# Optimization experiments

Hardware: AMD Instinct MI355X
Metric: run time of the kernel (lower is better)

## Reference

```python
import jax, jax.numpy as jnp
import numpy as np

N_HEADS = 16
D_QK = 64
D_MODEL = 1024
LN_EPS = 1e-6
B, QL, KVL = 2, 2048, 2048


def rms_norm(x, weight, eps=LN_EPS):
    var = jnp.mean(jnp.square(x.astype(jnp.float32)), axis=-1, keepdims=True)
    return (x * jax.lax.rsqrt(var + eps)).astype(x.dtype) * weight


def setup_inputs() -> dict:
    key = jax.random.key(0)
    ks = jax.random.split(key, 5)
    scale_h = 1.0 / np.sqrt(D_MODEL)
    return {
        "q_hidden_states": jax.random.normal(ks[0], (B, QL, D_MODEL), jnp.float32),
        "q_sequence_mask": jnp.ones((B, QL), dtype=bool),
        "kv_hidden_states": jax.random.normal(ks[1], (B, KVL, D_MODEL), jnp.float32),
        "kv_sequence_mask": jnp.ones((B, KVL), dtype=bool),
        "w_q": jax.random.normal(ks[2], (D_MODEL, N_HEADS * D_QK), jnp.float32) * scale_h,
        "w_kv": jax.random.normal(ks[3], (D_MODEL, 2 * N_HEADS * D_QK), jnp.float32) * scale_h,
        "w_o": jax.random.normal(ks[4], (N_HEADS * D_QK, D_MODEL), jnp.float32) * scale_h,
        "ln_weight": jnp.ones((D_MODEL,), jnp.float32),
    }


def reference(q_hidden_states, q_sequence_mask, kv_hidden_states, kv_sequence_mask,
              w_q, w_kv, w_o, ln_weight):
    b, ql, _ = q_hidden_states.shape
    kvl = kv_hidden_states.shape[1]

    normed = rms_norm(q_hidden_states, ln_weight)

    # q projection: [b, ql, H*D] -> [b, H, ql, D]
    q = (normed @ w_q).reshape(b, ql, N_HEADS, D_QK).transpose(0, 2, 1, 3)
    # kv projection: [b, kvl, 2*H*D] -> k, v each [b, H, kvl, D]
    kv = (kv_hidden_states @ w_kv).reshape(b, kvl, 2, N_HEADS, D_QK)
    k = kv[:, :, 0].transpose(0, 2, 1, 3)
    v = kv[:, :, 1].transpose(0, 2, 1, 3)

    # T5 attention: no 1/sqrt(d) scaling
    scores = jnp.einsum("bhqd,bhkd->bhqk", q, k)  # [b, H, ql, kvl]
    attn_mask = q_sequence_mask[:, None, :, None] & kv_sequence_mask[:, None, None, :]
    scores = jnp.where(attn_mask, scores, jnp.finfo(jnp.float32).min)
    attn = jax.nn.softmax(scores.astype(jnp.float32), axis=-1).astype(q.dtype)

    out = jnp.einsum("bhqk,bhkd->bhqd", attn, v)  # [b, H, ql, D]
    out = out.transpose(0, 2, 1, 3).reshape(b, ql, N_HEADS * D_QK)
    out = out @ w_o
    return q_hidden_states + out
```

## Files before the change

### kernel.cpp

```cpp
#include <hip/hip_runtime.h>
#include <stdint.h>

#define BSZ 2
#define QL 2048
#define KVL 2048
#define NH 16
#define DQK 64
#define DM 1024

typedef __bf16 bf16x8 __attribute__((ext_vector_type(8)));
typedef float f32x4 __attribute__((ext_vector_type(4)));

__device__ __forceinline__ ushort f2bf(float f) {
    union { float f; uint32_t u; } c; c.f = f;
    uint32_t u = c.u;
    return (ushort)((u + 0x7fffu + ((u >> 16) & 1u)) >> 16);
}

__device__ __forceinline__ uint32_t pack2bf(float lo, float hi) {
    union { float f; uint32_t u; } a, b;
    a.f = lo; b.f = hi;
    return __builtin_amdgcn_perm(b.u + 0x8000u, a.u + 0x8000u, 0x07060302u);
}

#define GLOAD_LDS16(g, l)                                              \
    __builtin_amdgcn_global_load_lds(                                  \
        (const __attribute__((address_space(1))) uint32_t*)(g),        \
        (__attribute__((address_space(3))) uint32_t*)(l), 16, 0, 0)

__global__ __launch_bounds__(256) void rmsnorm_cast_k(const float* __restrict__ x,
                                                      const float* __restrict__ w,
                                                      ushort* __restrict__ out) {
    int row = blockIdx.x;
    const float4* xr = (const float4*)(x + (size_t)row * DM);
    float4 v = xr[threadIdx.x];
    float s = v.x * v.x + v.y * v.y + v.z * v.z + v.w * v.w;
#pragma unroll
    for (int off = 32; off > 0; off >>= 1) s += __shfl_down(s, off, 64);
    __shared__ float ws4[4];
    if ((threadIdx.x & 63) == 0) ws4[threadIdx.x >> 6] = s;
    __syncthreads();
    float tot = ws4[0] + ws4[1] + ws4[2] + ws4[3];
    float r = rsqrtf(tot * (1.0f / DM) + 1e-6f);
    float4 wv = ((const float4*)w)[threadIdx.x];
    ushort4 o;
    o.x = f2bf(v.x * r * wv.x);
    o.y = f2bf(v.y * r * wv.y);
    o.z = f2bf(v.z * r * wv.z);
    o.w = f2bf(v.w * r * wv.w);
    ((ushort4*)(out + (size_t)row * DM))[threadIdx.x] = o;
}

__global__ __launch_bounds__(256) void prep_k(const float* __restrict__ kv_in,
                                              ushort* __restrict__ kvb,
                                              const float* __restrict__ w_q,
                                              const float* __restrict__ w_kv,
                                              const float* __restrict__ w_o,
                                              ushort* __restrict__ wqT,
                                              ushort* __restrict__ wkvT,
                                              ushort* __restrict__ woT) {
    __shared__ ushort tile[64][65];
    int blk = blockIdx.x;
    int tid = threadIdx.x;
    if (blk < 4096) {
        int i = blk * 256 + tid;
        float4 v = ((const float4*)kv_in)[i];
        ushort4 r;
        r.x = f2bf(v.x); r.y = f2bf(v.y); r.z = f2bf(v.z); r.w = f2bf(v.w);
        ((ushort4*)kvb)[i] = r;
        return;
    }
    int bi = blk - 4096;
    const float* in; ushort* out; int N, bx, by;
    const int K = 1024;
    if (bi < 256)      { in = w_q;  out = wqT;  N = 1024; bx = bi & 15; by = bi >> 4; }
    else if (bi < 768) { int j = bi - 256; in = w_kv; out = wkvT; N = 2048; bx = j & 31; by = j >> 5; }
    else               { int j = bi - 768; in = w_o;  out = woT;  N = 1024; bx = j & 15; by = j >> 4; }
    int k0 = by * 64, n0 = bx * 64;
    int colBase = tid & 63;
    int rowOff = tid >> 6;
#pragma unroll
    for (int i = 0; i < 16; ++i) {
        int row = i * 4 + rowOff;
        tile[colBase][row] = f2bf(in[(size_t)(k0 + row) * N + n0 + colBase]);
    }
    __syncthreads();
#pragma unroll
    for (int i = 0; i < 16; ++i) {
        int nrow = i * 4 + rowOff;
        out[(size_t)(n0 + nrow) * K + k0 + colBase] = tile[nrow][colBase];
    }
}

__global__ __launch_bounds__(256) void transpose_v_k(const ushort* __restrict__ v,
                                                     ushort* __restrict__ vt) {
    int bh = blockIdx.y;
    int t0 = blockIdx.x * 64;
    int lane = threadIdx.x & 63, wave = threadIdx.x >> 6;
    const ushort* src = v + (size_t)bh * KVL * DQK;
    ushort* dst = vt + (size_t)bh * DQK * KVL;
    int t = t0 + lane;
    int tp = (t & ~28) | ((t & 16) >> 2) | ((t & 4) << 1) | ((t & 8) << 1);
#pragma unroll
    for (int it = 0; it < 2; ++it) {
        int d0 = (wave * 2 + it) * 8;
        union { uint4 u; ushort s[8]; } val;
        val.u = *(const uint4*)&src[(size_t)t * DQK + d0];
#pragma unroll
        for (int j = 0; j < 8; ++j)
            dst[(size_t)(d0 + j) * KVL + tp] = val.s[j];
    }
}

__global__ __launch_bounds__(256) void gemm_qkv_k(
    const ushort* __restrict__ normed, const ushort* __restrict__ kvb,
    const ushort* __restrict__ wqT, const ushort* __restrict__ wkvT,
    ushort* __restrict__ q_out, ushort* __restrict__ k_out, ushort* __restrict__ v_out) {
    __shared__ __align__(16) ushort As[128 * 32];
    __shared__ __align__(16) ushort Bs[128 * 32];
    const int K = DM;
    int tid = threadIdx.x;
    int wave = tid >> 6, lane = tid & 63, quad = lane >> 4, l16 = lane & 15;
    int bx = blockIdx.x;
    int isQ = bx < 8;
    const ushort* A = isQ ? normed : kvb;
    const ushort* Bt = isQ ? wqT : wkvT;
    int n0 = (isQ ? bx : bx - 8) * 128;
    int m0 = blockIdx.y * 128;
    int wm = (wave & 1) * 64, wn = (wave >> 1) * 64;

    int r0 = tid >> 2, c0 = (tid & 3) << 3;
    const ushort* ga0 = &A[(size_t)(m0 + r0) * K + c0];
    const ushort* gb0 = &Bt[(size_t)(n0 + r0) * K + c0];

    f32x4 zero = {0.f, 0.f, 0.f, 0.f};
    f32x4 acc[4][4];
#pragma unroll
    for (int i = 0; i < 4; ++i)
#pragma unroll
        for (int j = 0; j < 4; ++j) acc[i][j] = zero;

    for (int k0 = 0; k0 < K; k0 += 32) {
        GLOAD_LDS16(ga0 + k0, &As[tid * 8]);
        GLOAD_LDS16(ga0 + (size_t)64 * K + k0, &As[(tid + 256) * 8]);
        GLOAD_LDS16(gb0 + k0, &Bs[tid * 8]);
        GLOAD_LDS16(gb0 + (size_t)64 * K + k0, &Bs[(tid + 256) * 8]);
        __syncthreads();
        bf16x8 af[4], bfr[4];
#pragma unroll
        for (int mi = 0; mi < 4; ++mi)
            af[mi] = *(const bf16x8*)(&As[(wm + mi * 16 + l16) * 32 + quad * 8]);
#pragma unroll
        for (int ni = 0; ni < 4; ++ni)
            bfr[ni] = *(const bf16x8*)(&Bs[(wn + ni * 16 + l16) * 32 + quad * 8]);
#pragma unroll
        for (int mi = 0; mi < 4; ++mi)
#pragma unroll
            for (int ni = 0; ni < 4; ++ni)
                acc[mi][ni] = __builtin_amdgcn_mfma_f32_16x16x32_bf16(
                    af[mi], bfr[ni], acc[mi][ni], 0, 0, 0);
        __syncthreads();
    }

    const float L2E = 1.44269504089f;
#pragma unroll
    for (int mi = 0; mi < 4; ++mi) {
#pragma unroll
        for (int ni = 0; ni < 4; ++ni) {
#pragma unroll
            for (int r = 0; r < 4; ++r) {
                int mm = m0 + wm + mi * 16 + quad * 4 + r;
                int nn = n0 + wn + ni * 16 + l16;
                float val = acc[mi][ni][r];
                int b = mm >> 11, t = mm & 2047;
                if (isQ) {
                    int h = nn >> 6, d = nn & 63;
                    q_out[((size_t)((b << 4) | h) * QL + t) * DQK + d] = f2bf(val * L2E);
                } else {
                    int c = nn >> 10, h = (nn >> 6) & 15, d = nn & 63;
                    ushort* dst = c ? v_out : k_out;
                    dst[((size_t)((b << 4) | h) * KVL + t) * DQK + d] = f2bf(val);
                }
            }
        }
    }
}

__global__ __launch_bounds__(256) void gemm_o_k(const ushort* __restrict__ A,
                                                const ushort* __restrict__ Bt,
                                                const float* __restrict__ resid,
                                                float* __restrict__ f_out) {
    __shared__ __align__(16) ushort As[64 * 32];
    __shared__ __align__(16) ushort Bs[128 * 32];
    const int K = DM;
    int tid = threadIdx.x;
    int wave = tid >> 6, lane = tid & 63, quad = lane >> 4, l16 = lane & 15;
    int n0 = blockIdx.x * 128, m0 = blockIdx.y * 64;
    int wm = (wave & 1) * 32, wn = (wave >> 1) * 64;

    int r0 = tid >> 2, c0 = (tid & 3) << 3;
    const ushort* ga0 = &A[(size_t)(m0 + r0) * K + c0];
    const ushort* gb0 = &Bt[(size_t)(n0 + r0) * K + c0];

    f32x4 zero = {0.f, 0.f, 0.f, 0.f};
    f32x4 acc[2][4];
#pragma unroll
    for (int i = 0; i < 2; ++i)
#pragma unroll
        for (int j = 0; j < 4; ++j) acc[i][j] = zero;

    for (int k0 = 0; k0 < K; k0 += 32) {
        GLOAD_LDS16(ga0 + k0, &As[tid * 8]);
        GLOAD_LDS16(gb0 + k0, &Bs[tid * 8]);
        GLOAD_LDS16(gb0 + (size_t)64 * K + k0, &Bs[(tid + 256) * 8]);
        __syncthreads();
        bf16x8 af[2], bfr[4];
#pragma unroll
        for (int mi = 0; mi < 2; ++mi)
            af[mi] = *(const bf16x8*)(&As[(wm + mi * 16 + l16) * 32 + quad * 8]);
#pragma unroll
        for (int ni = 0; ni < 4; ++ni)
            bfr[ni] = *(const bf16x8*)(&Bs[(wn + ni * 16 + l16) * 32 + quad * 8]);
#pragma unroll
        for (int mi = 0; mi < 2; ++mi)
#pragma unroll
            for (int ni = 0; ni < 4; ++ni)
                acc[mi][ni] = __builtin_amdgcn_mfma_f32_16x16x32_bf16(
                    af[mi], bfr[ni], acc[mi][ni], 0, 0, 0);
        __syncthreads();
    }

#pragma unroll
    for (int mi = 0; mi < 2; ++mi) {
#pragma unroll
        for (int ni = 0; ni < 4; ++ni) {
#pragma unroll
            for (int r = 0; r < 4; ++r) {
                int mm = m0 + wm + mi * 16 + quad * 4 + r;
                int nn = n0 + wn + ni * 16 + l16;
                size_t o = (size_t)mm * DM + nn;
                f_out[o] = resid[o] + acc[mi][ni][r];
            }
        }
    }
}

__global__ __launch_bounds__(256) void attn_k(const ushort* __restrict__ qh,
                                              const ushort* __restrict__ kh,
                                              const ushort* __restrict__ vt,
                                              ushort* __restrict__ ao) {
    __shared__ __align__(16) ushort smem[2 * 64 * 72];
    ushort* Ks = smem;
    ushort* Vs = smem + 64 * 72;
    int bh = blockIdx.y, bI = bh >> 4, hI = bh & 15;
    int q0 = blockIdx.x * 128;
    int tid = threadIdx.x, wave = tid >> 6, lane = tid & 63;
    int quad = lane >> 4, l16 = lane & 15;
    const ushort* Qp = qh + (size_t)bh * QL * DQK;
    const ushort* Kp = kh + (size_t)bh * KVL * DQK;
    const ushort* Vp = vt + (size_t)bh * DQK * KVL;

    bf16x8 qf[2][2];
#pragma unroll
    for (int g = 0; g < 2; ++g) {
        const ushort* qrow = Qp + (size_t)(q0 + wave * 32 + g * 16 + l16) * DQK;
        qf[g][0] = *(const bf16x8*)(qrow + quad * 8);
        qf[g][1] = *(const bf16x8*)(qrow + 32 + quad * 8);
    }

    int srow = tid >> 3;
    int scol = (tid & 7) << 3;

    f32x4 zero = {0.f, 0.f, 0.f, 0.f};
    f32x4 o[2][4];
#pragma unroll
    for (int g = 0; g < 2; ++g)
#pragma unroll
        for (int i = 0; i < 4; ++i) o[g][i] = zero;
    float lsum[2] = {0.f, 0.f};

    uint4 kr0 = *(const uint4*)&Kp[(size_t)srow * DQK + scol];
    uint4 kr1 = *(const uint4*)&Kp[(size_t)(srow + 32) * DQK + scol];
    uint4 vr0 = *(const uint4*)&Vp[(size_t)srow * KVL + scol];
    uint4 vr1 = *(const uint4*)&Vp[(size_t)(srow + 32) * KVL + scol];

    for (int t0 = 0; t0 < KVL; t0 += 64) {
        *(uint4*)&Ks[srow * 72 + scol] = kr0;
        *(uint4*)&Ks[(srow + 32) * 72 + scol] = kr1;
        *(uint4*)&Vs[srow * 72 + scol] = vr0;
        *(uint4*)&Vs[(srow + 32) * 72 + scol] = vr1;
        __syncthreads();
        int tn = t0 + 64;
        if (tn < KVL) {
            kr0 = *(const uint4*)&Kp[(size_t)(tn + srow) * DQK + scol];
            kr1 = *(const uint4*)&Kp[(size_t)(tn + srow + 32) * DQK + scol];
            vr0 = *(const uint4*)&Vp[(size_t)srow * KVL + tn + scol];
            vr1 = *(const uint4*)&Vp[(size_t)(srow + 32) * KVL + tn + scol];
        }

        f32x4 s[2][4];
#pragma unroll
        for (int mi = 0; mi < 4; ++mi) {
            const ushort* kb = &Ks[(mi * 16 + l16) * 72 + quad * 8];
            bf16x8 kf0 = *(const bf16x8*)kb;
            bf16x8 kf1 = *(const bf16x8*)(kb + 32);
#pragma unroll
            for (int g = 0; g < 2; ++g) {
                f32x4 a = zero;
                a = __builtin_amdgcn_mfma_f32_16x16x32_bf16(kf0, qf[g][0], a, 0, 0, 0);
                a = __builtin_amdgcn_mfma_f32_16x16x32_bf16(kf1, qf[g][1], a, 0, 0, 0);
                s[g][mi] = a;
            }
        }

        bf16x8 pf[2][2];
#pragma unroll
        for (int g = 0; g < 2; ++g) {
            float rs = 0.f;
            uint32_t pw[8];
#pragma unroll
            for (int mi = 0; mi < 4; ++mi) {
                float e0 = __builtin_amdgcn_exp2f(s[g][mi][0]);
                float e1 = __builtin_amdgcn_exp2f(s[g][mi][1]);
                float e2 = __builtin_amdgcn_exp2f(s[g][mi][2]);
                float e3 = __builtin_amdgcn_exp2f(s[g][mi][3]);
                rs += (e0 + e1) + (e2 + e3);
                asm("v_cvt_pk_bf16_f32 %0, %1, %2" : "=v"(pw[mi * 2]) : "v"(e0), "v"(e1));
                asm("v_cvt_pk_bf16_f32 %0, %1, %2" : "=v"(pw[mi * 2 + 1]) : "v"(e2), "v"(e3));
            }
            lsum[g] += rs;
            union { uint32_t u[4]; bf16x8 v; } b0, b1;
            b0.u[0] = pw[0]; b0.u[1] = pw[1]; b0.u[2] = pw[2]; b0.u[3] = pw[3];
            b1.u[0] = pw[4]; b1.u[1] = pw[5]; b1.u[2] = pw[6]; b1.u[3] = pw[7];
            pf[g][0] = b0.v;
            pf[g][1] = b1.v;
        }

#pragma unroll
        for (int mi = 0; mi < 4; ++mi) {
            const ushort* vb = &Vs[(mi * 16 + l16) * 72 + quad * 8];
            bf16x8 vf0 = *(const bf16x8*)vb;
            bf16x8 vf1 = *(const bf16x8*)(vb + 32);
#pragma unroll
            for (int g = 0; g < 2; ++g) {
                o[g][mi] = __builtin_amdgcn_mfma_f32_16x16x32_bf16(vf0, pf[g][0], o[g][mi], 0, 0, 0);
                o[g][mi] = __builtin_amdgcn_mfma_f32_16x16x32_bf16(vf1, pf[g][1], o[g][mi], 0, 0, 0);
            }
        }
        __syncthreads();
    }

#pragma unroll
    for (int g = 0; g < 2; ++g) {
        float lg = lsum[g];
        lg += __shfl_xor(lg, 16, 64);
        lg += __shfl_xor(lg, 32, 64);
        float rinv = __builtin_amdgcn_rcpf(lg);
        ushort* orow = &smem[(size_t)(wave * 32 + g * 16 + l16) * 72];
#pragma unroll
        for (int mi = 0; mi < 4; ++mi) {
            uint2 pk;
            pk.x = pack2bf(o[g][mi][0] * rinv, o[g][mi][1] * rinv);
            pk.y = pack2bf(o[g][mi][2] * rinv, o[g][mi][3] * rinv);
            *(uint2*)&orow[mi * 16 + quad * 4] = pk;
        }
    }
    __syncthreads();
#pragma unroll
    for (int it = 0; it < 4; ++it) {
        int idx = tid + it * 256;
        int ql = idx >> 3, c = (idx & 7) << 3;
        uint4 vv = *(const uint4*)&smem[ql * 72 + c];
        *(uint4*)&ao[((size_t)(bI * QL + q0 + ql)) * DM + hI * 64 + c] = vv;
    }
}

extern "C" void kernel_launch(void* const* d_in, const int* in_sizes, int n_in,
                              void* d_out, int out_size, void* d_ws, size_t ws_size,
                              hipStream_t stream) {
    (void)in_sizes; (void)n_in; (void)out_size; (void)ws_size;
    const float* qh_in = (const float*)d_in[0];
    const float* kv_in = (const float*)d_in[2];
    const float* w_q  = (const float*)d_in[4];
    const float* w_kv = (const float*)d_in[5];
    const float* w_o  = (const float*)d_in[6];
    const float* lnw  = (const float*)d_in[7];
    float* out = (float*)d_out;

    char* ws = (char*)d_ws;
    ushort* normed = (ushort*)(ws);
    ushort* vT     = (ushort*)(ws);
    ushort* kvb    = (ushort*)(ws + ((size_t)8 << 20));
    ushort* wqT    = (ushort*)(ws + ((size_t)16 << 20));
    ushort* wkvT   = (ushort*)(ws + ((size_t)18 << 20));
    ushort* woT    = (ushort*)(ws + ((size_t)22 << 20));
    ushort* qheads = (ushort*)(ws + ((size_t)24 << 20));
    ushort* kheads = (ushort*)(ws + ((size_t)32 << 20));
    ushort* vheads = (ushort*)(ws + ((size_t)40 << 20));
    ushort* attno  = (ushort*)(ws + ((size_t)48 << 20));

    rmsnorm_cast_k<<<BSZ * QL, 256, 0, stream>>>(qh_in, lnw, normed);
    prep_k<<<4096 + 1024, 256, 0, stream>>>(kv_in, kvb, w_q, w_kv, w_o, wqT, wkvT, woT);

    gemm_qkv_k<<<dim3(24, 32), 256, 0, stream>>>(normed, kvb, wqT, wkvT,
                                                 qheads, kheads, vheads);
    transpose_v_k<<<dim3(KVL / 64, BSZ * NH), 256, 0, stream>>>(vheads, vT);
    attn_k<<<dim3(QL / 128, BSZ * NH), 256, 0, stream>>>(qheads, kheads, vT, attno);
    gemm_o_k<<<dim3(8, 64), 256, 0, stream>>>(attno, woT, qh_in, out);
}
```

Measured before the change: 207.7 us.

## Load attention K/V fragments directly from global memory, dropping LDS staging and barriers

The attention kernel no longer stages K and V tiles through shared memory with two barriers per iteration. Each wave now loads its MFMA fragments for K and V straight from global memory into registers, software-prefetching the next K tile. The goal is to remove LDS traffic and block-level synchronisation. The cost is that every wave redundantly fetches the full K/V tiles (4x more global/L2 traffic per block) and uses more registers, partly offset by a launch-bounds hint for two blocks per SIMD-group.

After: 282.3 us. 35.9% more time.

```diff
diff --git a/kernel.cpp b/kernel.cpp
--- a/kernel.cpp
+++ b/kernel.cpp
@@ -245,13 +245,11 @@
     }
 }
 
-__global__ __launch_bounds__(256) void attn_k(const ushort* __restrict__ qh,
-                                              const ushort* __restrict__ kh,
-                                              const ushort* __restrict__ vt,
-                                              ushort* __restrict__ ao) {
-    __shared__ __align__(16) ushort smem[2 * 64 * 72];
-    ushort* Ks = smem;
-    ushort* Vs = smem + 64 * 72;
+__global__ __launch_bounds__(256, 2) void attn_k(const ushort* __restrict__ qh,
+                                                 const ushort* __restrict__ kh,
+                                                 const ushort* __restrict__ vt,
+                                                 ushort* __restrict__ ao) {
+    __shared__ __align__(16) ushort smem[128 * 72];
     int bh = blockIdx.y, bI = bh >> 4, hI = bh & 15;
     int q0 = blockIdx.x * 128;
     int tid = threadIdx.x, wave = tid >> 6, lane = tid & 63;
@@ -268,8 +266,8 @@
         qf[g][1] = *(const bf16x8*)(qrow + 32 + quad * 8);
     }
 
-    int srow = tid >> 3;
-    int scol = (tid & 7) << 3;
+    const ushort* kfb = Kp + (size_t)l16 * DQK + quad * 8;
+    const ushort* vfb = Vp + (size_t)l16 * KVL + quad * 8;
 
     f32x4 zero = {0.f, 0.f, 0.f, 0.f};
     f32x4 o[2][4];
@@ -279,36 +277,37 @@
         for (int i = 0; i < 4; ++i) o[g][i] = zero;
     float lsum[2] = {0.f, 0.f};
 
-    uint4 kr0 = *(const uint4*)&Kp[(size_t)srow * DQK + scol];
-    uint4 kr1 = *(const uint4*)&Kp[(size_t)(srow + 32) * DQK + scol];
-    uint4 vr0 = *(const uint4*)&Vp[(size_t)srow * KVL + scol];
-    uint4 vr1 = *(const uint4*)&Vp[(size_t)(srow + 32) * KVL + scol];
+    bf16x8 kc[4][2], kn[4][2];
+#pragma unroll
+    for (int mi = 0; mi < 4; ++mi) {
+        kc[mi][0] = *(const bf16x8*)(kfb + (size_t)(mi * 16) * DQK);
+        kc[mi][1] = *(const bf16x8*)(kfb + (size_t)(mi * 16) * DQK + 32);
+    }
 
     for (int t0 = 0; t0 < KVL; t0 += 64) {
-        *(uint4*)&Ks[srow * 72 + scol] = kr0;
-        *(uint4*)&Ks[(srow + 32) * 72 + scol] = kr1;
-        *(uint4*)&Vs[srow * 72 + scol] = vr0;
-        *(uint4*)&Vs[(srow + 32) * 72 + scol] = vr1;
-        __syncthreads();
+        bf16x8 vc[4][2];
+#pragma unroll
+        for (int mi = 0; mi < 4; ++mi) {
+            vc[mi][0] = *(const bf16x8*)(vfb + (size_t)(mi * 16) * KVL + t0);
+            vc[mi][1] = *(const bf16x8*)(vfb + (size_t)(mi * 16) * KVL + t0 + 32);
+        }
         int tn = t0 + 64;
         if (tn < KVL) {
-            kr0 = *(const uint4*)&Kp[(size_t)(tn + srow) * DQK + scol];
-            kr1 = *(const uint4*)&Kp[(size_t)(tn + srow + 32) * DQK + scol];
-            vr0 = *(const uint4*)&Vp[(size_t)srow * KVL + tn + scol];
-            vr1 = *(const uint4*)&Vp[(size_t)(srow + 32) * KVL + tn + scol];
+#pragma unroll
+            for (int mi = 0; mi < 4; ++mi) {
+                kn[mi][0] = *(const bf16x8*)(kfb + (size_t)(tn + mi * 16) * DQK);
+                kn[mi][1] = *(const bf16x8*)(kfb + (size_t)(tn + mi * 16) * DQK + 32);
+            }
         }
 
         f32x4 s[2][4];
 #pragma unroll
         for (int mi = 0; mi < 4; ++mi) {
-            const ushort* kb = &Ks[(mi * 16 + l16) * 72 + quad * 8];
-            bf16x8 kf0 = *(const bf16x8*)kb;
-            bf16x8 kf1 = *(const bf16x8*)(kb + 32);
 #pragma unroll
             for (int g = 0; g < 2; ++g) {
                 f32x4 a = zero;
-                a = __builtin_amdgcn_mfma_f32_16x16x32_bf16(kf0, qf[g][0], a, 0, 0, 0);
-                a = __builtin_amdgcn_mfma_f32_16x16x32_bf16(kf1, qf[g][1], a, 0, 0, 0);
+                a = __builtin_amdgcn_mfma_f32_16x16x32_bf16(kc[mi][0], qf[g][0], a, 0, 0, 0);
+                a = __builtin_amdgcn_mfma_f32_16x16x32_bf16(kc[mi][1], qf[g][1], a, 0, 0, 0);
                 s[g][mi] = a;
             }
         }
@@ -338,16 +337,18 @@
 
 #pragma unroll
         for (int mi = 0; mi < 4; ++mi) {
-            const ushort* vb = &Vs[(mi * 16 + l16) * 72 + quad * 8];
-            bf16x8 vf0 = *(const bf16x8*)vb;
-            bf16x8 vf1 = *(const bf16x8*)(vb + 32);
 #pragma unroll
             for (int g = 0; g < 2; ++g) {
-                o[g][mi] = __builtin_amdgcn_mfma_f32_16x16x32_bf16(vf0, pf[g][0], o[g][mi], 0, 0, 0);
-                o[g][mi] = __builtin_amdgcn_mfma_f32_16x16x32_bf16(vf1, pf[g][1], o[g][mi], 0, 0, 0);
-            }
-        }
-        __syncthreads();
+                o[g][mi] = __builtin_amdgcn_mfma_f32_16x16x32_bf16(vc[mi][0], pf[g][0], o[g][mi], 0, 0, 0);
+                o[g][mi] = __builtin_amdgcn_mfma_f32_16x16x32_bf16(vc[mi][1], pf[g][1], o[g][mi], 0, 0, 0);
+            }
+        }
+
+#pragma unroll
+        for (int mi = 0; mi < 4; ++mi) {
+            kc[mi][0] = kn[mi][0];
+            kc[mi][1] = kn[mi][1];
+        }
     }
 
 #pragma unroll
```

## Fuse V transpose into QKV GEMM epilogue and double-buffer attention K/V tiles

Applied to the files above, without the earlier changes.

The QKV GEMM epilogue now writes V directly in the transposed, permuted layout that attention expects, packing four bf16 values per store. This removes the separate transpose kernel and one round trip of V through global memory. The attention kernel also double-buffers its K/V shared-memory tiles, so the next tile is written after compute and one barrier per iteration is dropped. In exchange, shared memory per block doubles, which may lower occupancy, and the transposed V stores from the GEMM are strided.

Result: slower. 222.7 us (+7.2%).

```diff
diff --git a/kernel.cpp b/kernel.cpp
--- a/kernel.cpp
+++ b/kernel.cpp
@@ -92,30 +92,10 @@
     }
 }
 
-__global__ __launch_bounds__(256) void transpose_v_k(const ushort* __restrict__ v,
-                                                     ushort* __restrict__ vt) {
-    int bh = blockIdx.y;
-    int t0 = blockIdx.x * 64;
-    int lane = threadIdx.x & 63, wave = threadIdx.x >> 6;
-    const ushort* src = v + (size_t)bh * KVL * DQK;
-    ushort* dst = vt + (size_t)bh * DQK * KVL;
-    int t = t0 + lane;
-    int tp = (t & ~28) | ((t & 16) >> 2) | ((t & 4) << 1) | ((t & 8) << 1);
-#pragma unroll
-    for (int it = 0; it < 2; ++it) {
-        int d0 = (wave * 2 + it) * 8;
-        union { uint4 u; ushort s[8]; } val;
-        val.u = *(const uint4*)&src[(size_t)t * DQK + d0];
-#pragma unroll
-        for (int j = 0; j < 8; ++j)
-            dst[(size_t)(d0 + j) * KVL + tp] = val.s[j];
-    }
-}
-
 __global__ __launch_bounds__(256) void gemm_qkv_k(
     const ushort* __restrict__ normed, const ushort* __restrict__ kvb,
     const ushort* __restrict__ wqT, const ushort* __restrict__ wkvT,
-    ushort* __restrict__ q_out, ushort* __restrict__ k_out, ushort* __restrict__ v_out) {
+    ushort* __restrict__ q_out, ushort* __restrict__ k_out, ushort* __restrict__ vT) {
     __shared__ __align__(16) ushort As[128 * 32];
     __shared__ __align__(16) ushort Bs[128 * 32];
     const int K = DM;
@@ -167,19 +147,29 @@
     for (int mi = 0; mi < 4; ++mi) {
 #pragma unroll
         for (int ni = 0; ni < 4; ++ni) {
-#pragma unroll
-            for (int r = 0; r < 4; ++r) {
-                int mm = m0 + wm + mi * 16 + quad * 4 + r;
-                int nn = n0 + wn + ni * 16 + l16;
-                float val = acc[mi][ni][r];
-                int b = mm >> 11, t = mm & 2047;
-                if (isQ) {
-                    int h = nn >> 6, d = nn & 63;
-                    q_out[((size_t)((b << 4) | h) * QL + t) * DQK + d] = f2bf(val * L2E);
-                } else {
-                    int c = nn >> 10, h = (nn >> 6) & 15, d = nn & 63;
-                    ushort* dst = c ? v_out : k_out;
-                    dst[((size_t)((b << 4) | h) * KVL + t) * DQK + d] = f2bf(val);
+            int nn = n0 + wn + ni * 16 + l16;
+            if (!isQ && (nn >> 10)) {
+                int h = (nn >> 6) & 15, d = nn & 63;
+                int mm0 = m0 + wm + mi * 16 + quad * 4;
+                int b = mm0 >> 11, tb = mm0 & 2047;
+                int tp = (tb & ~28) | ((tb & 16) >> 2) | ((tb & 4) << 1) | ((tb & 8) << 1);
+                uint2 pk;
+                pk.x = pack2bf(acc[mi][ni][0], acc[mi][ni][1]);
+                pk.y = pack2bf(acc[mi][ni][2], acc[mi][ni][3]);
+                *(uint2*)&vT[((size_t)((b << 4) | h) * DQK + d) * KVL + tp] = pk;
+            } else {
+#pragma unroll
+                for (int r = 0; r < 4; ++r) {
+                    int mm = m0 + wm + mi * 16 + quad * 4 + r;
+                    float val = acc[mi][ni][r];
+                    int b = mm >> 11, t = mm & 2047;
+                    if (isQ) {
+                        int h = nn >> 6, d = nn & 63;
+                        q_out[((size_t)((b << 4) | h) * QL + t) * DQK + d] = f2bf(val * L2E);
+                    } else {
+                        int h = (nn >> 6) & 15, d = nn & 63;
+                        k_out[((size_t)((b << 4) | h) * KVL + t) * DQK + d] = f2bf(val);
+                    }
                 }
             }
         }
@@ -249,9 +239,8 @@
                                               const ushort* __restrict__ kh,
                                               const ushort* __restrict__ vt,
                                               ushort* __restrict__ ao) {
-    __shared__ __align__(16) ushort smem[2 * 64 * 72];
-    ushort* Ks = smem;
-    ushort* Vs = smem + 64 * 72;
+    __shared__ __align__(16) ushort smem[4 * 64 * 72];
+    const int HALF = 64 * 72;
     int bh = blockIdx.y, bI = bh >> 4, hI = bh & 15;
     int q0 = blockIdx.x * 128;
     int tid = threadIdx.x, wave = tid >> 6, lane = tid & 63;
@@ -279,18 +268,27 @@
         for (int i = 0; i < 4; ++i) o[g][i] = zero;
     float lsum[2] = {0.f, 0.f};
 
-    uint4 kr0 = *(const uint4*)&Kp[(size_t)srow * DQK + scol];
-    uint4 kr1 = *(const uint4*)&Kp[(size_t)(srow + 32) * DQK + scol];
-    uint4 vr0 = *(const uint4*)&Vp[(size_t)srow * KVL + scol];
-    uint4 vr1 = *(const uint4*)&Vp[(size_t)(srow + 32) * KVL + scol];
-
+    {
+        uint4 a = *(const uint4*)&Kp[(size_t)srow * DQK + scol];
+        uint4 b = *(const uint4*)&Kp[(size_t)(srow + 32) * DQK + scol];
+        uint4 c = *(const uint4*)&Vp[(size_t)srow * KVL + scol];
+        uint4 d = *(const uint4*)&Vp[(size_t)(srow + 32) * KVL + scol];
+        *(uint4*)&smem[srow * 72 + scol] = a;
+        *(uint4*)&smem[(srow + 32) * 72 + scol] = b;
+        *(uint4*)&smem[HALF + srow * 72 + scol] = c;
+        *(uint4*)&smem[HALF + (srow + 32) * 72 + scol] = d;
+    }
+    __syncthreads();
+
+    int cur = 0;
     for (int t0 = 0; t0 < KVL; t0 += 64) {
-        *(uint4*)&Ks[srow * 72 + scol] = kr0;
-        *(uint4*)&Ks[(srow + 32) * 72 + scol] = kr1;
-        *(uint4*)&Vs[srow * 72 + scol] = vr0;
-        *(uint4*)&Vs[(srow + 32) * 72 + scol] = vr1;
-        __syncthreads();
+        ushort* Ks = smem + cur * 2 * HALF;
+        ushort* Vs = Ks + HALF;
+        ushort* Kn = smem + (cur ^ 1) * 2 * HALF;
+        ushort* Vn = Kn + HALF;
+
         int tn = t0 + 64;
+        uint4 kr0, kr1, vr0, vr1;
         if (tn < KVL) {
             kr0 = *(const uint4*)&Kp[(size_t)(tn + srow) * DQK + scol];
             kr1 = *(const uint4*)&Kp[(size_t)(tn + srow + 32) * DQK + scol];
@@ -347,7 +345,15 @@
                 o[g][mi] = __builtin_amdgcn_mfma_f32_16x16x32_bf16(vf1, pf[g][1], o[g][mi], 0, 0, 0);
             }
         }
+
+        if (tn < KVL) {
+            *(uint4*)&Kn[srow * 72 + scol] = kr0;
+            *(uint4*)&Kn[(srow + 32) * 72 + scol] = kr1;
+            *(uint4*)&Vn[srow * 72 + scol] = vr0;
+            *(uint4*)&Vn[(srow + 32) * 72 + scol] = vr1;
+        }
         __syncthreads();
+        cur ^= 1;
     }
 
 #pragma unroll
@@ -389,22 +395,20 @@
 
     char* ws = (char*)d_ws;
     ushort* normed = (ushort*)(ws);
-    ushort* vT     = (ushort*)(ws);
     ushort* kvb    = (ushort*)(ws + ((size_t)8 << 20));
     ushort* wqT    = (ushort*)(ws + ((size_t)16 << 20));
     ushort* wkvT   = (ushort*)(ws + ((size_t)18 << 20));
     ushort* woT    = (ushort*)(ws + ((size_t)22 << 20));
     ushort* qheads = (ushort*)(ws + ((size_t)24 << 20));
     ushort* kheads = (ushort*)(ws + ((size_t)32 << 20));
-    ushort* vheads = (ushort*)(ws + ((size_t)40 << 20));
+    ushort* vT     = (ushort*)(ws + ((size_t)40 << 20));
     ushort* attno  = (ushort*)(ws + ((size_t)48 << 20));
 
     rmsnorm_cast_k<<<BSZ * QL, 256, 0, stream>>>(qh_in, lnw, normed);
     prep_k<<<4096 + 1024, 256, 0, stream>>>(kv_in, kvb, w_q, w_kv, w_o, wqT, wkvT, woT);
 
     gemm_qkv_k<<<dim3(24, 32), 256, 0, stream>>>(normed, kvb, wqT, wkvT,
-                                                 qheads, kheads, vheads);
-    transpose_v_k<<<dim3(KVL / 64, BSZ * NH), 256, 0, stream>>>(vheads, vT);
+                                                 qheads, kheads, vT);
     attn_k<<<dim3(QL / 128, BSZ * NH), 256, 0, stream>>>(qheads, kheads, vT, attno);
     gemm_o_k<<<dim3(8, 64), 256, 0, stream>>>(attno, woT, qh_in, out);
 }
```

## Double-buffer LDS tiles in QKV and output projection GEMMs

Applied to the files above, without the earlier changes.

Both projection GEMM kernels now keep two shared-memory tile buffers and issue the global-to-LDS loads for the next K slice before computing on the current one. The aim is to hide global load latency behind MFMA work. Each K step still ends with a barrier, which orders the loads. LDS use per block doubles, which may lower occupancy.

Measured after the change: 211.2 us. No clear change (+1.7%).

```diff
diff --git a/kernel.cpp b/kernel.cpp
--- a/kernel.cpp
+++ b/kernel.cpp
@@ -116,8 +116,10 @@
     const ushort* __restrict__ normed, const ushort* __restrict__ kvb,
     const ushort* __restrict__ wqT, const ushort* __restrict__ wkvT,
     ushort* __restrict__ q_out, ushort* __restrict__ k_out, ushort* __restrict__ v_out) {
-    __shared__ __align__(16) ushort As[128 * 32];
-    __shared__ __align__(16) ushort Bs[128 * 32];
+    __shared__ __align__(16) ushort As0[128 * 32];
+    __shared__ __align__(16) ushort Bs0[128 * 32];
+    __shared__ __align__(16) ushort As1[128 * 32];
+    __shared__ __align__(16) ushort Bs1[128 * 32];
     const int K = DM;
     int tid = threadIdx.x;
     int wave = tid >> 6, lane = tid & 63, quad = lane >> 4, l16 = lane & 15;
@@ -140,27 +142,43 @@
 #pragma unroll
         for (int j = 0; j < 4; ++j) acc[i][j] = zero;
 
-    for (int k0 = 0; k0 < K; k0 += 32) {
-        GLOAD_LDS16(ga0 + k0, &As[tid * 8]);
-        GLOAD_LDS16(ga0 + (size_t)64 * K + k0, &As[(tid + 256) * 8]);
-        GLOAD_LDS16(gb0 + k0, &Bs[tid * 8]);
-        GLOAD_LDS16(gb0 + (size_t)64 * K + k0, &Bs[(tid + 256) * 8]);
-        __syncthreads();
-        bf16x8 af[4], bfr[4];
-#pragma unroll
-        for (int mi = 0; mi < 4; ++mi)
-            af[mi] = *(const bf16x8*)(&As[(wm + mi * 16 + l16) * 32 + quad * 8]);
-#pragma unroll
-        for (int ni = 0; ni < 4; ++ni)
-            bfr[ni] = *(const bf16x8*)(&Bs[(wn + ni * 16 + l16) * 32 + quad * 8]);
-#pragma unroll
-        for (int mi = 0; mi < 4; ++mi)
-#pragma unroll
-            for (int ni = 0; ni < 4; ++ni)
-                acc[mi][ni] = __builtin_amdgcn_mfma_f32_16x16x32_bf16(
-                    af[mi], bfr[ni], acc[mi][ni], 0, 0, 0);
-        __syncthreads();
-    }
+#define QKV_STAGE(kk, Ad, Bd)                                          \
+    do {                                                               \
+        GLOAD_LDS16(ga0 + (kk), &Ad[tid * 8]);                         \
+        GLOAD_LDS16(ga0 + (size_t)64 * K + (kk), &Ad[(tid + 256) * 8]);\
+        GLOAD_LDS16(gb0 + (kk), &Bd[tid * 8]);                         \
+        GLOAD_LDS16(gb0 + (size_t)64 * K + (kk), &Bd[(tid + 256) * 8]);\
+    } while (0)
+
+#define QKV_COMPUTE(Asrc, Bsrc)                                        \
+    do {                                                               \
+        bf16x8 af[4], bfr[4];                                          \
+        _Pragma("unroll")                                              \
+        for (int mi = 0; mi < 4; ++mi)                                 \
+            af[mi] = *(const bf16x8*)(&Asrc[(wm + mi * 16 + l16) * 32 + quad * 8]); \
+        _Pragma("unroll")                                              \
+        for (int ni = 0; ni < 4; ++ni)                                 \
+            bfr[ni] = *(const bf16x8*)(&Bsrc[(wn + ni * 16 + l16) * 32 + quad * 8]); \
+        _Pragma("unroll")                                              \
+        for (int mi = 0; mi < 4; ++mi)                                 \
+            _Pragma("unroll")                                          \
+            for (int ni = 0; ni < 4; ++ni)                             \
+                acc[mi][ni] = __builtin_amdgcn_mfma_f32_16x16x32_bf16( \
+                    af[mi], bfr[ni], acc[mi][ni], 0, 0, 0);            \
+    } while (0)
+
+    QKV_STAGE(0, As0, Bs0);
+    __syncthreads();
+    for (int k0 = 0; k0 < K; k0 += 64) {
+        QKV_STAGE(k0 + 32, As1, Bs1);
+        QKV_COMPUTE(As0, Bs0);
+        __syncthreads();
+        if (k0 + 64 < K) QKV_STAGE(k0 + 64, As0, Bs0);
+        QKV_COMPUTE(As1, Bs1);
+        __syncthreads();
+    }
+#undef QKV_STAGE
+#undef QKV_COMPUTE
 
     const float L2E = 1.44269504089f;
 #pragma unroll
@@ -190,8 +208,10 @@
                                                 const ushort* __restrict__ Bt,
                                                 const float* __restrict__ resid,
                                                 float* __restrict__ f_out) {
-    __shared__ __align__(16) ushort As[64 * 32];
-    __shared__ __align__(16) ushort Bs[128 * 32];
+    __shared__ __align__(16) ushort As0[64 * 32];
+    __shared__ __align__(16) ushort Bs0[128 * 32];
+    __shared__ __align__(16) ushort As1[64 * 32];
+    __shared__ __align__(16) ushort Bs1[128 * 32];
     const int K = DM;
     int tid = threadIdx.x;
     int wave = tid >> 6, lane = tid & 63, quad = lane >> 4, l16 = lane & 15;
@@ -209,26 +229,42 @@
 #pragma unroll
         for (int j = 0; j < 4; ++j) acc[i][j] = zero;
 
-    for (int k0 = 0; k0 < K; k0 += 32) {
-        GLOAD_LDS16(ga0 + k0, &As[tid * 8]);
-        GLOAD_LDS16(gb0 + k0, &Bs[tid * 8]);
-        GLOAD_LDS16(gb0 + (size_t)64 * K + k0, &Bs[(tid + 256) * 8]);
-        __syncthreads();
-        bf16x8 af[2], bfr[4];
-#pragma unroll
-        for (int mi = 0; mi < 2; ++mi)
-            af[mi] = *(const bf16x8*)(&As[(wm + mi * 16 + l16) * 32 + quad * 8]);
-#pragma unroll
-        for (int ni = 0; ni < 4; ++ni)
-            bfr[ni] = *(const bf16x8*)(&Bs[(wn + ni * 16 + l16) * 32 + quad * 8]);
-#pragma unroll
-        for (int mi = 0; mi < 2; ++mi)
-#pragma unroll
-            for (int ni = 0; ni < 4; ++ni)
-                acc[mi][ni] = __builtin_amdgcn_mfma_f32_16x16x32_bf16(
-                    af[mi], bfr[ni], acc[mi][ni], 0, 0, 0);
-        __syncthreads();
-    }
+#define O_STAGE(kk, Ad, Bd)                                            \
+    do {                                                               \
+        GLOAD_LDS16(ga0 + (kk), &Ad[tid * 8]);                         \
+        GLOAD_LDS16(gb0 + (kk), &Bd[tid * 8]);                         \
+        GLOAD_LDS16(gb0 + (size_t)64 * K + (kk), &Bd[(tid + 256) * 8]);\
+    } while (0)
+
+#define O_COMPUTE(Asrc, Bsrc)                                          \
+    do {                                                               \
+        bf16x8 af[2], bfr[4];                                          \
+        _Pragma("unroll")                                              \
+        for (int mi = 0; mi < 2; ++mi)                                 \
+            af[mi] = *(const bf16x8*)(&Asrc[(wm + mi * 16 + l16) * 32 + quad * 8]); \
+        _Pragma("unroll")                                              \
+        for (int ni = 0; ni < 4; ++ni)                                 \
+            bfr[ni] = *(const bf16x8*)(&Bsrc[(wn + ni * 16 + l16) * 32 + quad * 8]); \
+        _Pragma("unroll")                                              \
+        for (int mi = 0; mi < 2; ++mi)                                 \
+            _Pragma("unroll")                                          \
+            for (int ni = 0; ni < 4; ++ni)                             \
+                acc[mi][ni] = __builtin_amdgcn_mfma_f32_16x16x32_bf16( \
+                    af[mi], bfr[ni], acc[mi][ni], 0, 0, 0);            \
+    } while (0)
+
+    O_STAGE(0, As0, Bs0);
+    __syncthreads();
+    for (int k0 = 0; k0 < K; k0 += 64) {
+        O_STAGE(k0 + 32, As1, Bs1);
+        O_COMPUTE(As0, Bs0);
+        __syncthreads();
+        if (k0 + 64 < K) O_STAGE(k0 + 64, As0, Bs0);
+        O_COMPUTE(As1, Bs1);
+        __syncthreads();
+    }
+#undef O_STAGE
+#undef O_COMPUTE
 
 #pragma unroll
     for (int mi = 0; mi < 2; ++mi) {
```
